# Kernel tuning notes

Measured on AMD Instinct MI355X. Metric: run time of the kernel, lower is better.

The kernel has to match this reference:

```python
import jax, jax.numpy as jnp
import numpy as np

D = 384
H = 6
DK = D // H
EPS = 1e-5


def _layernorm(x, g, b):
    mu = jnp.mean(x, axis=-1, keepdims=True)
    var = jnp.var(x, axis=-1, keepdims=True)
    return (x - mu) * jax.lax.rsqrt(var + EPS) * g + b


def setup_inputs() -> dict:
    key = jax.random.key(0)
    ks = jax.random.split(key, 12)
    B, N = 8, 2048
    s = lambda fan_in: 1.0 / np.sqrt(fan_in)
    return {
        "points": jax.random.normal(ks[0], (B, 3 + D, N), dtype=jnp.float32),
        "ln1_g": jnp.ones((D,), jnp.float32),
        "ln1_b": jnp.zeros((D,), jnp.float32),
        "w_qkv": jax.random.uniform(ks[1], (3 * D, D), jnp.float32, -s(D), s(D)),
        "w_o": jax.random.uniform(ks[2], (D, D), jnp.float32, -s(D), s(D)),
        "b_o": jnp.zeros((D,), jnp.float32),
        "ln2_g": jnp.ones((D,), jnp.float32),
        "ln2_b": jnp.zeros((D,), jnp.float32),
        "w1": jax.random.uniform(ks[3], (2 * D, D), jnp.float32, -s(D), s(D)),
        "b1": jnp.zeros((2 * D,), jnp.float32),
        "w2": jax.random.uniform(ks[4], (D, 2 * D), jnp.float32, -s(2 * D), s(2 * D)),
        "b2": jnp.zeros((D,), jnp.float32),
    }


def reference(points, ln1_g, ln1_b, w_qkv, w_o, b_o, ln2_g, ln2_b, w1, b1, w2, b2):
    coords = points[:, :3, :]                       # [B, 3, N]
    feats = jnp.transpose(points[:, 3:, :], (0, 2, 1))  # [B, N, D]
    B, N, _ = feats.shape

    # pre-norm + fused QKV projection (no bias)
    h = _layernorm(feats, ln1_g, ln1_b)
    qkv = jnp.einsum('bnd,ed->bne', h, w_qkv)       # [B, N, 3D]
    q, k, v = jnp.split(qkv, 3, axis=-1)

    split_heads = lambda t: jnp.transpose(t.reshape(B, N, H, DK), (0, 2, 1, 3))
    q, k, v = split_heads(q), split_heads(k), split_heads(v)  # [B, H, N, DK]

    scale = DK ** -0.5
    scores = jnp.einsum('bhid,bhjd->bhij', q, k) * scale      # [B, H, N, N]
    attn = jax.nn.softmax(scores, axis=-1)
    ctx = jnp.einsum('bhij,bhjd->bhid', attn, v)              # [B, H, N, DK]
    ctx = jnp.transpose(ctx, (0, 2, 1, 3)).reshape(B, N, D)
    attn_out = jnp.einsum('bnd,ed->bne', ctx, w_o) + b_o

    x = feats + attn_out
    # FFN with exact (erf) GELU, hidden = 2*D
    h2 = _layernorm(x, ln2_g, ln2_b)
    ff = jnp.einsum('bnd,ed->bne', h2, w1) + b1
    ff = jax.nn.gelu(ff, approximate=False)
    ff = jnp.einsum('bne,de->bnd', ff, w2) + b2
    x = x + ff

    return jnp.concatenate([coords, jnp.transpose(x, (0, 2, 1))], axis=1)
```

## Files before the change

kernel.cpp:

```cpp
#include <hip/hip_runtime.h>
#include <cstdint>


typedef __bf16 bf16;
typedef __bf16 bf16x8 __attribute__((ext_vector_type(8)));
typedef __bf16 bf16x4 __attribute__((ext_vector_type(4)));
typedef short s16x4 __attribute__((ext_vector_type(4)));
typedef float floatx4 __attribute__((ext_vector_type(4)));
typedef uint32_t __attribute__((address_space(1))) gu32;
typedef uint32_t __attribute__((address_space(3))) lu32;

#define NN 2048
#define DD 384
#define HH 6
#define DK 64
#define BB 8
#define MM (BB * NN)
#define D3 (3 * DD)
#define D2 (2 * DD)
#define CH (3 + DD)
#define LP 72
#define LPV 136

#define QSCALE 0.18033688011112042f

static __device__ __forceinline__ s16x4 as_s16x4(bf16x4 v) {
    union { bf16x4 b; s16x4 s; } u; u.b = v; return u.s;
}


__global__ void cast_all_kernel(const float* __restrict__ w_qkv, const float* __restrict__ w_o,
                                const float* __restrict__ w1, const float* __restrict__ w2,
                                bf16* __restrict__ o_qkv, bf16* __restrict__ o_o,
                                bf16* __restrict__ o_w1, bf16* __restrict__ o_w2) {
    int i = blockIdx.x * 256 + threadIdx.x;
    if (i < 442368) o_qkv[i] = (bf16)w_qkv[i];
    else if (i < 589824) o_o[i - 442368] = (bf16)w_o[i - 442368];
    else if (i < 884736) o_w1[i - 589824] = (bf16)w1[i - 589824];
    else o_w2[i - 884736] = (bf16)w2[i - 884736];
}

__global__ __launch_bounds__(256) void pre_kernel(const float* __restrict__ pts,
                                                  const float* __restrict__ g,
                                                  const float* __restrict__ bta,
                                                  float* __restrict__ feats,
                                                  bf16* __restrict__ h1,
                                                  float* __restrict__ out) {
    __shared__ float T[32][385];
    const int b = blockIdx.y, n0 = blockIdx.x * 32;
    const int t = threadIdx.x;
    const float* src = pts + (size_t)b * CH * NN;

    if (t < 96) {
        const int r = t >> 5, n = t & 31;
        out[((size_t)b * CH + r) * NN + n0 + n] = src[(size_t)r * NN + n0 + n];
    }

    const int n = t & 31, d0 = t >> 5;
#pragma unroll
    for (int p = 0; p < 48; ++p) {
        const int d = p * 8 + d0;
        T[n][d] = src[(size_t)(3 + d) * NN + n0 + n];
    }
    __syncthreads();

    const int wave = t >> 6, lane = t & 63;
#pragma unroll
    for (int i = 0; i < 8; ++i) {
        const int rn = wave * 8 + i;
        float v[6], s = 0.f, sq = 0.f;
#pragma unroll
        for (int j = 0; j < 6; ++j) { v[j] = T[rn][lane + j * 64]; s += v[j]; sq += v[j] * v[j]; }
#pragma unroll
        for (int o = 1; o < 64; o <<= 1) { s += __shfl_xor(s, o); sq += __shfl_xor(sq, o); }
        const float mu = s * (1.f / DD);
        const float var = sq * (1.f / DD) - mu * mu;
        const float rs = rsqrtf(var + 1e-5f);
        float* fr = feats + ((size_t)b * NN + n0 + rn) * DD;
        bf16* hr = h1 + ((size_t)b * NN + n0 + rn) * DD;
#pragma unroll
        for (int j = 0; j < 6; ++j) {
            const int d = lane + j * 64;
            fr[d] = v[j];
            hr[d] = (bf16)((v[j] - mu) * rs * g[d] + bta[d]);
        }
    }
}

__global__ __launch_bounds__(256) void ln_kernel(const float* __restrict__ x,
                                                 const float* __restrict__ g,
                                                 const float* __restrict__ bta,
                                                 bf16* __restrict__ out) {
    int wave = threadIdx.x >> 6, lane = threadIdx.x & 63;
    int row = blockIdx.x * 4 + wave;
    const float* xr = x + (size_t)row * DD;
    float v[6], s = 0.f, sq = 0.f;
#pragma unroll
    for (int i = 0; i < 6; ++i) { v[i] = xr[lane + i * 64]; s += v[i]; sq += v[i] * v[i]; }
#pragma unroll
    for (int o = 1; o < 64; o <<= 1) { s += __shfl_xor(s, o); sq += __shfl_xor(sq, o); }
    float mu = s * (1.f / DD);
    float var = sq * (1.f / DD) - mu * mu;
    float rs = rsqrtf(var + 1e-5f);
    bf16* orow = out + (size_t)row * DD;
#pragma unroll
    for (int i = 0; i < 6; ++i) {
        int d = lane + i * 64;
        orow[d] = (bf16)((v[i] - mu) * rs * g[d] + bta[d]);
    }
}

template <int NC, int K, int MODE, int TN>
__global__ __launch_bounds__(256, 2)
void gemm_bt(const bf16* __restrict__ A, const bf16* __restrict__ W,
             const float* __restrict__ bias, const float* __restrict__ res,
             bf16* __restrict__ obf, float* __restrict__ of32, bf16* __restrict__ vt) {
    constexpr int MI = (TN == 128) ? 4 : 2;
    __shared__ bf16 As[128 * 64];
    __shared__ bf16 Ws[TN * 64];
    const int t = threadIdx.x;
    const int wave = t >> 6, lane = t & 63;
    const int m0 = blockIdx.x * 128, n0 = blockIdx.y * TN;
    const int wm = (TN == 128) ? (wave >> 1) * 64 : wave * 32;
    const int wn = (TN == 128) ? (wave & 1) * 64 : 0;
    const int lr = lane & 15, quad = lane >> 4, lx = lane & 7;

    const int srow = t >> 3;
    const int schunk = ((t & 7) ^ (srow & 7)) * 8;

    const int ca0 = ((quad) ^ lx) * 16;
    const int ca1 = ((4 + quad) ^ lx) * 16;
    const int arow = (wm + lr) * 128;
    const int brow = (wn + lr) * 128;

    floatx4 acc[MI][4];
#pragma unroll
    for (int mi = 0; mi < MI; ++mi)
#pragma unroll
        for (int ni = 0; ni < 4; ++ni) {
            floatx4 z = {0.f, 0.f, 0.f, 0.f};
            acc[mi][ni] = z;
        }

    for (int k0 = 0; k0 < K; k0 += 64) {
        __syncthreads();
#pragma unroll
        for (int i = 0; i < 4; ++i) {
            const int r = i * 32 + srow;
            __builtin_amdgcn_global_load_lds(
                (const gu32*)&A[(size_t)(m0 + r) * K + k0 + schunk],
                (lu32*)&As[i * 2048 + t * 8], 16, 0, 0);
        }
#pragma unroll
        for (int i = 0; i < TN / 32; ++i) {
            const int r = i * 32 + srow;
            __builtin_amdgcn_global_load_lds(
                (const gu32*)&W[(size_t)(n0 + r) * K + k0 + schunk],
                (lu32*)&Ws[i * 2048 + t * 8], 16, 0, 0);
        }
        __syncthreads();

        const char* ab = (const char*)As;
        const char* wb = (const char*)Ws;
#pragma unroll
        for (int kk = 0; kk < 2; ++kk) {
            const int ca = kk ? ca1 : ca0;
            bf16x8 af[MI], bfr[4];
#pragma unroll
            for (int mi = 0; mi < MI; ++mi)
                af[mi] = *(const bf16x8*)(ab + arow + mi * 2048 + ca);
#pragma unroll
            for (int ni = 0; ni < 4; ++ni)
                bfr[ni] = *(const bf16x8*)(wb + brow + ni * 2048 + ca);
#pragma unroll
            for (int mi = 0; mi < MI; ++mi)
#pragma unroll
                for (int ni = 0; ni < 4; ++ni)
                    acc[mi][ni] = __builtin_amdgcn_mfma_f32_16x16x32_bf16(af[mi], bfr[ni], acc[mi][ni], 0, 0, 0);
        }
    }

#pragma unroll
    for (int mi = 0; mi < MI; ++mi) {
#pragma unroll
        for (int ni = 0; ni < 4; ++ni) {
            const int r0 = m0 + wm + mi * 16 + quad * 4;
            const int c = n0 + wn + ni * 16 + lr;
            floatx4 v = acc[mi][ni];
            if constexpr (MODE == 0) {
                const int cb = n0 + wn + ni * 16;
                if (cb >= 2 * DD) {
                    const int hh = (c - 2 * DD) >> 6, dk = (c - 2 * DD) & 63;
                    const int b = r0 >> 11, n = r0 & (NN - 1);
                    bf16x4 pk;
#pragma unroll
                    for (int r = 0; r < 4; ++r) pk[r] = (bf16)v[r];
                    *(bf16x4*)&vt[((size_t)(b * HH + hh) * DK + dk) * NN + n] = pk;
                } else {
                    const float sc_q = (cb < DD) ? QSCALE : 1.0f;
#pragma unroll
                    for (int r = 0; r < 4; ++r) obf[(size_t)(r0 + r) * NC + c] = (bf16)(v[r] * sc_q);
                }
            } else if constexpr (MODE == 1) {
#pragma unroll
                for (int r = 0; r < 4; ++r)
                    of32[(size_t)(r0 + r) * NC + c] = v[r] + bias[c] + res[(size_t)(r0 + r) * NC + c];
            } else if constexpr (MODE == 2) {
#pragma unroll
                for (int r = 0; r < 4; ++r) {
                    float u = v[r] + bias[c];
                    obf[(size_t)(r0 + r) * NC + c] = (bf16)(0.5f * u * (1.f + erff(u * 0.70710678118f)));
                }
            } else {
                const int b = r0 >> 11, n = r0 & (NN - 1);
                float o4[4];
#pragma unroll
                for (int r = 0; r < 4; ++r)
                    o4[r] = v[r] + bias[c] + res[(size_t)(r0 + r) * DD + c];
                float4 val = make_float4(o4[0], o4[1], o4[2], o4[3]);
                *(float4*)&of32[((size_t)b * CH + 3 + c) * NN + n] = val;
            }
        }
    }
}

__global__ __launch_bounds__(256, 3)
void attn_kernel(const bf16* __restrict__ qkv, const bf16* __restrict__ vt,
                 bf16* __restrict__ ctx) {
    __shared__ bf16 Ks[128 * LP];
    __shared__ bf16 Vs[64 * LPV];
    const int t = threadIdx.x, wave = t >> 6, lane = t & 63;
    const int lr = lane & 15, quad = lane >> 4;
    const int bh = blockIdx.y, b = bh / HH, h = bh % HH;
    const int q0 = blockIdx.x * 128 + wave * 32;
    const bf16* qbase = qkv + (size_t)b * NN * D3 + h * DK;
    const bf16* kbase = qbase + DD;
    const bf16* vbase = vt + (size_t)bh * DK * NN;

    bf16x8 aq[2][2];
#pragma unroll
    for (int mi = 0; mi < 2; ++mi)
#pragma unroll
        for (int ks = 0; ks < 2; ++ks)
            aq[mi][ks] = *(const bf16x8*)&qbase[(size_t)(q0 + mi * 16 + lr) * D3 +
                                                ks * 32 + quad * 8];

    bf16x4 ones4;
#pragma unroll
    for (int i = 0; i < 4; ++i) ones4[i] = (bf16)1.0f;
    const s16x4 ones_s = as_s16x4(ones4);

    floatx4 o[2][4], ol[2];
#pragma unroll
    for (int mi = 0; mi < 2; ++mi) {
        floatx4 z = {0.f, 0.f, 0.f, 0.f};
        ol[mi] = z;
#pragma unroll
        for (int nd = 0; nd < 4; ++nd) o[mi][nd] = z;
    }

    for (int j0 = 0; j0 < NN; j0 += 128) {
        __syncthreads();
        {
            const int rr = t >> 3, cc = (t & 7) * 8;
#pragma unroll
            for (int i = 0; i < 4; ++i) {
                const int j = i * 32 + rr;
                *(bf16x8*)&Ks[j * LP + cc] =
                    *(const bf16x8*)&kbase[(size_t)(j0 + j) * D3 + cc];
            }
            const int rr2 = t >> 4, cc2 = (t & 15) * 8;
#pragma unroll
            for (int i = 0; i < 4; ++i) {
                const int d = i * 16 + rr2;
                *(bf16x8*)&Vs[d * LPV + cc2] =
                    *(const bf16x8*)&vbase[(size_t)d * NN + j0 + cc2];
            }
        }
        __syncthreads();

        floatx4 s[2][8];
#pragma unroll
        for (int mi = 0; mi < 2; ++mi)
#pragma unroll
            for (int nj = 0; nj < 8; ++nj) {
                floatx4 z = {0.f, 0.f, 0.f, 0.f};
                s[mi][nj] = z;
            }
#pragma unroll
        for (int ks = 0; ks < 2; ++ks)
#pragma unroll
            for (int nj = 0; nj < 8; ++nj) {
                bf16x8 bk = *(const bf16x8*)&Ks[(nj * 16 + lr) * LP + ks * 32 + quad * 8];
#pragma unroll
                for (int mi = 0; mi < 2; ++mi)
                    s[mi][nj] = __builtin_amdgcn_mfma_f32_16x16x32_bf16(bk, aq[mi][ks],
                                                                        s[mi][nj], 0, 0, 0);
            }

#pragma unroll
        for (int nj = 0; nj < 8; ++nj) {
            s16x4 ap[2];
#pragma unroll
            for (int mi = 0; mi < 2; ++mi) {
                bf16x4 pk;
#pragma unroll
                for (int r = 0; r < 4; ++r) pk[r] = (bf16)exp2f(s[mi][nj][r]);
                ap[mi] = as_s16x4(pk);
            }
#pragma unroll
            for (int nd = 0; nd < 4; ++nd) {
                s16x4 bv = as_s16x4(*(const bf16x4*)&Vs[(nd * 16 + lr) * LPV +
                                                        nj * 16 + quad * 4]);
#pragma unroll
                for (int mi = 0; mi < 2; ++mi)
                    o[mi][nd] = __builtin_amdgcn_mfma_f32_16x16x16bf16_1k(ap[mi], bv,
                                                                          o[mi][nd], 0, 0, 0);
            }
#pragma unroll
            for (int mi = 0; mi < 2; ++mi)
                ol[mi] = __builtin_amdgcn_mfma_f32_16x16x16bf16_1k(ap[mi], ones_s, ol[mi], 0, 0, 0);
        }
    }

#pragma unroll
    for (int mi = 0; mi < 2; ++mi)
#pragma unroll
        for (int r = 0; r < 4; ++r) {
            const int n = q0 + mi * 16 + quad * 4 + r;
            const float inv = 1.0f / ol[mi][r];
#pragma unroll
            for (int nd = 0; nd < 4; ++nd) {
                const int d = h * DK + nd * 16 + lr;
                ctx[(size_t)(b * NN + n) * DD + d] = (bf16)(o[mi][nd][r] * inv);
            }
        }
}


extern "C" void kernel_launch(void* const* d_in, const int* in_sizes, int n_in,
                              void* d_out, int out_size, void* d_ws, size_t ws_size,
                              hipStream_t stream) {
    const float* points = (const float*)d_in[0];
    const float* ln1_g = (const float*)d_in[1];
    const float* ln1_b = (const float*)d_in[2];
    const float* w_qkv = (const float*)d_in[3];
    const float* w_o   = (const float*)d_in[4];
    const float* b_o   = (const float*)d_in[5];
    const float* ln2_g = (const float*)d_in[6];
    const float* ln2_b = (const float*)d_in[7];
    const float* w1    = (const float*)d_in[8];
    const float* b1    = (const float*)d_in[9];
    const float* w2    = (const float*)d_in[10];
    const float* b2    = (const float*)d_in[11];
    float* out = (float*)d_out;

    char* ws = (char*)d_ws;
    size_t off = 0;
    auto alloc = [&](size_t bytes) -> void* {
        void* p = ws + off;
        off += (bytes + 255) & ~(size_t)255;
        return p;
    };
    float* feats = (float*)alloc((size_t)MM * DD * 4);
    float* xbuf  = (float*)alloc((size_t)MM * DD * 4);
    bf16* h1     = (bf16*)alloc((size_t)MM * DD * 2);
    bf16* h2     = (bf16*)alloc((size_t)MM * DD * 2);
    bf16* qkvb   = (bf16*)alloc((size_t)MM * D3 * 2);
    bf16* vtb    = (bf16*)alloc((size_t)BB * HH * DK * NN * 2);
    bf16* ctx    = (bf16*)alloc((size_t)MM * DD * 2);
    bf16* ffh    = (bf16*)alloc((size_t)MM * D2 * 2);
    bf16* wqkv_bf = (bf16*)alloc((size_t)D3 * DD * 2);
    bf16* wo_bf   = (bf16*)alloc((size_t)DD * DD * 2);
    bf16* w1_bf   = (bf16*)alloc((size_t)D2 * DD * 2);
    bf16* w2_bf   = (bf16*)alloc((size_t)DD * D2 * 2);

    cast_all_kernel<<<1179648 / 256, 256, 0, stream>>>(w_qkv, w_o, w1, w2,
                                                       wqkv_bf, wo_bf, w1_bf, w2_bf);
    pre_kernel<<<dim3(NN / 32, BB), 256, 0, stream>>>(points, ln1_g, ln1_b,
                                                      feats, h1, out);
    gemm_bt<D3, DD, 0, 128><<<dim3(MM / 128, D3 / 128), 256, 0, stream>>>(
        h1, wqkv_bf, nullptr, nullptr, qkvb, nullptr, vtb);
    attn_kernel<<<dim3(NN / 128, BB * HH), 256, 0, stream>>>(qkvb, vtb, ctx);
    gemm_bt<DD, DD, 1, 64><<<dim3(MM / 128, DD / 64), 256, 0, stream>>>(
        ctx, wo_bf, b_o, feats, nullptr, xbuf, nullptr);
    ln_kernel<<<MM / 4, 256, 0, stream>>>(xbuf, ln2_g, ln2_b, h2);
    gemm_bt<D2, DD, 2, 128><<<dim3(MM / 128, D2 / 128), 256, 0, stream>>>(
        h2, w1_bf, b1, nullptr, ffh, nullptr, nullptr);
    gemm_bt<DD, D2, 3, 64><<<dim3(MM / 128, DD / 64), 256, 0, stream>>>(
        ffh, w2_bf, b2, xbuf, nullptr, out, nullptr);
}
```

Baseline: 276.6 us.

## Drop feats buffer, read residual from points via LDS transpose; fuse weight cast

The pre kernel no longer writes the fp32 transposed feats copy. The out-projection GEMM instead reads the residual straight from the channel-major points tensor and transposes it through shared memory before the epilogue add. The weight-cast kernel is folded into the pre kernel as extra blocks, which saves one launch. In exchange the MODE 1 GEMM gets two extra barriers and a larger shared-memory footprint.

```diff
diff --git a/kernel.cpp b/kernel.cpp
--- a/kernel.cpp
+++ b/kernel.cpp
@@ -22,33 +22,40 @@
 #define LP 72
 #define LPV 136
 
+#define PREBLK (BB * NN / 32)
+#define CASTBLK 576
+
 #define QSCALE 0.18033688011112042f
 
 static __device__ __forceinline__ s16x4 as_s16x4(bf16x4 v) {
     union { bf16x4 b; s16x4 s; } u; u.b = v; return u.s;
 }
 
-
-__global__ void cast_all_kernel(const float* __restrict__ w_qkv, const float* __restrict__ w_o,
-                                const float* __restrict__ w1, const float* __restrict__ w2,
-                                bf16* __restrict__ o_qkv, bf16* __restrict__ o_o,
-                                bf16* __restrict__ o_w1, bf16* __restrict__ o_w2) {
-    int i = blockIdx.x * 256 + threadIdx.x;
-    if (i < 442368) o_qkv[i] = (bf16)w_qkv[i];
-    else if (i < 589824) o_o[i - 442368] = (bf16)w_o[i - 442368];
-    else if (i < 884736) o_w1[i - 589824] = (bf16)w1[i - 589824];
-    else o_w2[i - 884736] = (bf16)w2[i - 884736];
-}
-
-__global__ __launch_bounds__(256) void pre_kernel(const float* __restrict__ pts,
-                                                  const float* __restrict__ g,
-                                                  const float* __restrict__ bta,
-                                                  float* __restrict__ feats,
-                                                  bf16* __restrict__ h1,
-                                                  float* __restrict__ out) {
+__global__ __launch_bounds__(256) void pre_kernel(
+        const float* __restrict__ pts, const float* __restrict__ g,
+        const float* __restrict__ bta, bf16* __restrict__ h1,
+        float* __restrict__ out,
+        const float* __restrict__ w_qkv, const float* __restrict__ w_o,
+        const float* __restrict__ w1, const float* __restrict__ w2,
+        bf16* __restrict__ o_qkv, bf16* __restrict__ o_o,
+        bf16* __restrict__ o_w1, bf16* __restrict__ o_w2) {
     __shared__ float T[32][385];
-    const int b = blockIdx.y, n0 = blockIdx.x * 32;
-    const int t = threadIdx.x;
+    const int bid = blockIdx.x, t = threadIdx.x;
+
+    if (bid >= PREBLK) {
+        const int base = (bid - PREBLK) * 2048 + t * 8;
+#pragma unroll
+        for (int i = 0; i < 8; ++i) {
+            const int idx = base + i;
+            if (idx < 442368) o_qkv[idx] = (bf16)w_qkv[idx];
+            else if (idx < 589824) o_o[idx - 442368] = (bf16)w_o[idx - 442368];
+            else if (idx < 884736) o_w1[idx - 589824] = (bf16)w1[idx - 589824];
+            else o_w2[idx - 884736] = (bf16)w2[idx - 884736];
+        }
+        return;
+    }
+
+    const int b = bid >> 6, n0 = (bid & 63) * 32;
     const float* src = pts + (size_t)b * CH * NN;
 
     if (t < 96) {
@@ -76,12 +83,10 @@
         const float mu = s * (1.f / DD);
         const float var = sq * (1.f / DD) - mu * mu;
         const float rs = rsqrtf(var + 1e-5f);
-        float* fr = feats + ((size_t)b * NN + n0 + rn) * DD;
         bf16* hr = h1 + ((size_t)b * NN + n0 + rn) * DD;
 #pragma unroll
         for (int j = 0; j < 6; ++j) {
             const int d = lane + j * 64;
-            fr[d] = v[j];
             hr[d] = (bf16)((v[j] - mu) * rs * g[d] + bta[d]);
         }
     }
@@ -116,8 +121,13 @@
              const float* __restrict__ bias, const float* __restrict__ res,
              bf16* __restrict__ obf, float* __restrict__ of32, bf16* __restrict__ vt) {
     constexpr int MI = (TN == 128) ? 4 : 2;
-    __shared__ bf16 As[128 * 64];
-    __shared__ bf16 Ws[TN * 64];
+    constexpr int SMEM_KLOOP = (128 * 64 + TN * 64) * 2;
+    constexpr int SMEM_RT = 64 * 132 * 4;
+    constexpr int SMEM_BYTES =
+        (MODE == 1 && SMEM_RT > SMEM_KLOOP) ? SMEM_RT : SMEM_KLOOP;
+    __shared__ __align__(16) char smem[SMEM_BYTES];
+    bf16* As = (bf16*)smem;
+    bf16* Ws = (bf16*)(smem + 128 * 64 * 2);
     const int t = threadIdx.x;
     const int wave = t >> 6, lane = t & 63;
     const int m0 = blockIdx.x * 128, n0 = blockIdx.y * TN;
@@ -178,6 +188,20 @@
                 for (int ni = 0; ni < 4; ++ni)
                     acc[mi][ni] = __builtin_amdgcn_mfma_f32_16x16x32_bf16(af[mi], bfr[ni], acc[mi][ni], 0, 0, 0);
         }
+    }
+
+    float* Rt = (float*)smem;
+    if constexpr (MODE == 1) {
+        __syncthreads();
+        const int bb = m0 >> 11, m0n = m0 & (NN - 1);
+        const int cc = t >> 2, l4 = (t & 3) * 32;
+        const float* prow = res + ((size_t)bb * CH + 3 + n0 + cc) * NN + m0n + l4;
+#pragma unroll
+        for (int i = 0; i < 8; ++i) {
+            float4 vv = *(const float4*)&prow[i * 4];
+            *(float4*)&Rt[cc * 132 + l4 + i * 4] = vv;
+        }
+        __syncthreads();
     }
 
 #pragma unroll
@@ -202,9 +226,11 @@
                     for (int r = 0; r < 4; ++r) obf[(size_t)(r0 + r) * NC + c] = (bf16)(v[r] * sc_q);
                 }
             } else if constexpr (MODE == 1) {
+                const int rr = (wn + ni * 16 + lr) * 132;
+                const int nnb = wm + mi * 16 + quad * 4;
 #pragma unroll
                 for (int r = 0; r < 4; ++r)
-                    of32[(size_t)(r0 + r) * NC + c] = v[r] + bias[c] + res[(size_t)(r0 + r) * NC + c];
+                    of32[(size_t)(r0 + r) * NC + c] = v[r] + bias[c] + Rt[rr + nnb + r];
             } else if constexpr (MODE == 2) {
 #pragma unroll
                 for (int r = 0; r < 4; ++r) {
@@ -362,7 +388,6 @@
         off += (bytes + 255) & ~(size_t)255;
         return p;
     };
-    float* feats = (float*)alloc((size_t)MM * DD * 4);
     float* xbuf  = (float*)alloc((size_t)MM * DD * 4);
     bf16* h1     = (bf16*)alloc((size_t)MM * DD * 2);
     bf16* h2     = (bf16*)alloc((size_t)MM * DD * 2);
@@ -375,15 +400,14 @@
     bf16* w1_bf   = (bf16*)alloc((size_t)D2 * DD * 2);
     bf16* w2_bf   = (bf16*)alloc((size_t)DD * D2 * 2);
 
-    cast_all_kernel<<<1179648 / 256, 256, 0, stream>>>(w_qkv, w_o, w1, w2,
-                                                       wqkv_bf, wo_bf, w1_bf, w2_bf);
-    pre_kernel<<<dim3(NN / 32, BB), 256, 0, stream>>>(points, ln1_g, ln1_b,
-                                                      feats, h1, out);
+    pre_kernel<<<PREBLK + CASTBLK, 256, 0, stream>>>(
+        points, ln1_g, ln1_b, h1, out,
+        w_qkv, w_o, w1, w2, wqkv_bf, wo_bf, w1_bf, w2_bf);
     gemm_bt<D3, DD, 0, 128><<<dim3(MM / 128, D3 / 128), 256, 0, stream>>>(
         h1, wqkv_bf, nullptr, nullptr, qkvb, nullptr, vtb);
     attn_kernel<<<dim3(NN / 128, BB * HH), 256, 0, stream>>>(qkvb, vtb, ctx);
     gemm_bt<DD, DD, 1, 64><<<dim3(MM / 128, DD / 64), 256, 0, stream>>>(
-        ctx, wo_bf, b_o, feats, nullptr, xbuf, nullptr);
+        ctx, wo_bf, b_o, points, nullptr, xbuf, nullptr);
     ln_kernel<<<MM / 4, 256, 0, stream>>>(xbuf, ln2_g, ln2_b, h2);
     gemm_bt<D2, DD, 2, 128><<<dim3(MM / 128, D2 / 128), 256, 0, stream>>>(
         h2, w1_bf, b1, nullptr, ffh, nullptr, nullptr);
```

Result: no change. 274.9 us, median of 3 (-0.6%).
